# Performance work log

Measured on AMD Instinct MI355X. Metric: run time of the kernel, lower is better.

The kernel has to match this reference:

```python
import jax, jax.numpy as jnp
import numpy as np

# static sizes
B = 32          # graphs
NPER = 1024     # nodes per graph
N0 = B * NPER
F_IN = 128
H = 4           # heads
DH = 32         # per-head dim (128/4)
HID = H * DH    # 128
E = 524288      # edges (avg degree 16)
K1, K2, K3 = 512, 256, 128  # ceil(0.5*nper) per stage
NC = 10


def gcn_agg(h, src, dst, w, n):
    """GCNConv propagation: sym-normalized aggregation with self-loops.
    h: [n,F] already projected; w: [E] edge weight (0 for filtered edges)."""
    deg = jax.ops.segment_sum(w, dst, num_segments=n) + 1.0  # +1 self-loop
    dinv = jax.lax.rsqrt(deg)
    coef = dinv[src] * dinv[dst] * w                          # [E]
    agg = jax.ops.segment_sum(h[src] * coef[:, None], dst, num_segments=n)
    return agg + h / deg[:, None]  # self-loop term: dinv[i]^2 = 1/deg[i]


def mh_gcn(x, W, b, src, dst, w, n):
    """MAGPoolGCNLayer: per-head GCNConv (32->32), relu, concat heads."""
    h = jnp.einsum('nhd,hde->nhe', x.reshape(n, H, DH), W).reshape(n, HID)
    return jax.nn.relu(gcn_agg(h, src, dst, w, n) + b.reshape(HID))


def att_pool(x, src, dst, w, A, psW, psb, n, k):
    """MultiHeadAtt: standard att, complex score, concat pooling, global weight."""
    sub = x.reshape(n, H, DH)
    att = jnp.einsum('nhd,hd->nh', sub, A)            # per-head Linear(32,1)
    cat = (att[:, :, None] * sub).reshape(n, HID)     # score*sub, concat
    score = (gcn_agg(cat @ psW, src, dst, w, n) + psb)[:, 0]  # GCNConv(HID,1)
    nper = n // B
    _, idx = jax.lax.top_k(score.reshape(B, nper), k)  # per-graph topk
    perm = (idx + jnp.arange(B)[:, None] * nper).reshape(-1)
    xn = x[perm] * jnp.tanh(score[perm])[:, None]      # global att weighting
    # filter_adj: remap kept nodes, mask edges touching dropped nodes
    nmap = jnp.full((n,), -1, jnp.int32).at[perm].set(jnp.arange(B * k, dtype=jnp.int32))
    ns, nd = nmap[src], nmap[dst]
    wn = w * ((ns >= 0) & (nd >= 0)).astype(w.dtype)
    return xn, jnp.maximum(ns, 0), jnp.maximum(nd, 0), wn


def readout(x):
    # graphs are contiguous with equal node counts -> reshape readout
    xr = x.reshape(B, -1, x.shape[-1])
    return jnp.concatenate([xr.max(1), xr.mean(1)], axis=1)  # [B, 2*HID]


def setup_inputs():
    key = jax.random.key(0)
    ks = jax.random.split(key, 26)
    gid = jnp.repeat(jnp.arange(B, dtype=jnp.int32), E // B)
    src = jax.random.randint(ks[0], (E,), 0, NPER, dtype=jnp.int32) + gid * NPER
    dst = jax.random.randint(ks[1], (E,), 0, NPER, dtype=jnp.int32) + gid * NPER
    x = jax.random.normal(ks[2], (N0, F_IN), jnp.float32)
    s = 0.1
    def rn(k, shp):
        return jax.random.normal(k, shp, jnp.float32) * s
    return {
        'x': x, 'src': src, 'dst': dst,
        'W1': rn(ks[3], (H, DH, DH)), 'b1': rn(ks[4], (H, DH)), 'A1': rn(ks[5], (H, DH)),
        'ps1W': rn(ks[6], (HID, 1)), 'ps1b': rn(ks[7], (1,)),
        'W2': rn(ks[8], (H, DH, DH)), 'b2': rn(ks[9], (H, DH)), 'A2': rn(ks[10], (H, DH)),
        'ps2W': rn(ks[11], (HID, 1)), 'ps2b': rn(ks[12], (1,)),
        'W3': rn(ks[13], (H, DH, DH)), 'b3': rn(ks[14], (H, DH)), 'A3': rn(ks[15], (H, DH)),
        'ps3W': rn(ks[16], (HID, 1)), 'ps3b': rn(ks[17], (1,)),
        'l1W': rn(ks[18], (2 * HID, HID)), 'l1b': rn(ks[19], (HID,)),
        'l2W': rn(ks[20], (HID, HID // 2)), 'l2b': rn(ks[21], (HID // 2,)),
        'l3W': rn(ks[22], (HID // 2, NC)), 'l3b': rn(ks[23], (NC,)),
    }


def reference(x, src, dst, W1, b1, A1, ps1W, ps1b, W2, b2, A2, ps2W, ps2b,
              W3, b3, A3, ps3W, ps3b, l1W, l1b, l2W, l2b, l3W, l3b):
    w = jnp.ones((E,), x.dtype)
    h = mh_gcn(x, W1, b1, src, dst, w, N0)
    h, s1, d1, w1 = att_pool(h, src, dst, w, A1, ps1W, ps1b, N0, K1)
    r1 = readout(h)
    n1 = B * K1
    h = mh_gcn(h, W2, b2, s1, d1, w1, n1)
    h, s2, d2, w2 = att_pool(h, s1, d1, w1, A2, ps2W, ps2b, n1, K2)
    r2 = readout(h)
    n2 = B * K2
    h = mh_gcn(h, W3, b3, s2, d2, w2, n2)
    h, _, _, _ = att_pool(h, s2, d2, w2, A3, ps3W, ps3b, n2, K3)
    r3 = readout(h)
    z = r1 + r2 + r3                      # [B, 2*HID]
    z = jax.nn.relu(z @ l1W + l1b)        # dropout skipped (eval mode)
    z = jax.nn.relu(z @ l2W + l2b)
    return jax.nn.log_softmax(z @ l3W + l3b, axis=-1)
```

## Files before the change

### kernel.cpp

```cpp
#include <hip/hip_runtime.h>
#include <math.h>

#define BGR 32
#define NPER0 1024
#define N0 (BGR * NPER0)
#define FDIM 128
#define EDG 524288
#define K1 512
#define K2 256
#define K3 128
#define EBLK (EDG / 256)
#define SXP 36
#define CAP 64

__device__ __forceinline__ unsigned enc_f(float v) {
    unsigned u = __float_as_uint(v);
    return (u & 0x80000000u) ? ~u : (u | 0x80000000u);
}
__device__ __forceinline__ float dec_f(unsigned u) {
    return (u & 0x80000000u) ? __uint_as_float(u ^ 0x80000000u) : __uint_as_float(~u);
}

__global__ void zero_all(int* __restrict__ cntA, int* __restrict__ cntB,
                         int* __restrict__ cntC, unsigned* __restrict__ rmax,
                         float* __restrict__ rsum) {
    int i = blockIdx.x * 256 + threadIdx.x;
    if (i < N0) cntA[i] = 0;
    if (i < BGR * K1) cntB[i] = 0;
    if (i < BGR * K2) cntC[i] = 0;
    if (i < 3 * BGR * FDIM) { rmax[i] = 0u; rsum[i] = 0.0f; }
}

__device__ __forceinline__ void proj_compute(float* __restrict__ hp, int nb, int t,
                                             const float* __restrict__ sW,
                                             const float* __restrict__ sxT) {
    const int fg = t >> 3, ng = t & 7, h = fg >> 3;
    const float* ap = sxT + h * 32 * SXP + ng * 4;
    const float* bp = sW + h * 1024 + (fg & 7) * 4;
    float4 acc0 = {0.f, 0.f, 0.f, 0.f}, acc1 = acc0, acc2 = acc0, acc3 = acc0;
#pragma unroll
    for (int k = 0; k < 32; k++) {
        float4 a = *(const float4*)(ap + k * SXP);
        float4 b = *(const float4*)(bp + k * 32);
        acc0.x = fmaf(a.x, b.x, acc0.x); acc0.y = fmaf(a.x, b.y, acc0.y);
        acc0.z = fmaf(a.x, b.z, acc0.z); acc0.w = fmaf(a.x, b.w, acc0.w);
        acc1.x = fmaf(a.y, b.x, acc1.x); acc1.y = fmaf(a.y, b.y, acc1.y);
        acc1.z = fmaf(a.y, b.z, acc1.z); acc1.w = fmaf(a.y, b.w, acc1.w);
        acc2.x = fmaf(a.z, b.x, acc2.x); acc2.y = fmaf(a.z, b.y, acc2.y);
        acc2.z = fmaf(a.z, b.z, acc2.z); acc2.w = fmaf(a.z, b.w, acc2.w);
        acc3.x = fmaf(a.w, b.x, acc3.x); acc3.y = fmaf(a.w, b.y, acc3.y);
        acc3.z = fmaf(a.w, b.z, acc3.z); acc3.w = fmaf(a.w, b.w, acc3.w);
    }
    float4* op = (float4*)(hp + (size_t)(nb + ng * 4) * FDIM + fg * 4);
    op[0] = acc0; op[32] = acc1; op[64] = acc2; op[96] = acc3;
}

__device__ __forceinline__ void pool_body(const float* __restrict__ ha,
                                          const int* __restrict__ perm,
                                          const float* __restrict__ mult, int k, int pb,
                                          unsigned* __restrict__ rmax,
                                          float* __restrict__ rsum,
                                          float* __restrict__ smax,
                                          float* __restrict__ ssum) {
    const int t = threadIdx.x;
    const int g = pb & 31;
    const int c = pb >> 5;
    const int f = t & 127, half = t >> 7;
    const int base = g * k + c * 8;
    float vmax = -1e30f, vsum = 0.0f;
#pragma unroll
    for (int j0 = 0; j0 < 4; j0++) {
        int newid = base + half + j0 * 2;
        int old = perm[newid];
        float m = mult[newid];
        float v = ha[(size_t)old * FDIM + f] * m;
        vmax = fmaxf(vmax, v);
        vsum += v;
    }
    if (half) { smax[f] = vmax; ssum[f] = vsum; }
    __syncthreads();
    if (!half) {
        vmax = fmaxf(vmax, smax[f]);
        vsum += ssum[f];
        atomicMax(&rmax[g * FDIM + f], enc_f(vmax));
        atomicAdd(&rsum[g * FDIM + f], vsum);
    }
}

__global__ void bin_proj1(const int* __restrict__ src, const int* __restrict__ dst,
                          int* __restrict__ cnt, int* __restrict__ slot,
                          const float* __restrict__ x, const float* __restrict__ W,
                          float* __restrict__ hp) {
    __shared__ __align__(16) float sW[4096];
    __shared__ __align__(16) float sxT[128 * SXP];
    const int t = threadIdx.x;
    if (blockIdx.x < EBLK) {
        int e = blockIdx.x * 256 + t;
        int s = src[e];
        int d = dst[e];
        int p = atomicAdd(&cnt[d], 1);
        if (p < CAP) slot[d * CAP + p] = s;
        return;
    }
    const int nb = (blockIdx.x - EBLK) * 32;
    for (int i = t; i < 4096; i += 256) sW[i] = W[i];
    for (int i = t; i < 4096; i += 256) {
        int node = i >> 7, dim = i & 127;
        sxT[dim * SXP + node] = x[(size_t)(nb + node) * FDIM + dim];
    }
    __syncthreads();
    proj_compute(hp, nb, t, sW, sxT);
}

__global__ void bin_proj_pool(const int* __restrict__ src0, const int* __restrict__ dst0,
                              const int* __restrict__ nmapA, const int* __restrict__ nmapB,
                              int* __restrict__ cnt_next, int* __restrict__ slot_next,
                              const float* __restrict__ ha, const int* __restrict__ perm,
                              const float* __restrict__ mult, const float* __restrict__ W,
                              float* __restrict__ hp, int ntiles, int kprev,
                              unsigned* __restrict__ rmax, float* __restrict__ rsum) {
    __shared__ __align__(16) float sW[4096];
    __shared__ __align__(16) float sxT[128 * SXP];
    const int t = threadIdx.x;
    if (blockIdx.x < EBLK) {
        int e = blockIdx.x * 256 + t;
        int a = nmapA[src0[e]];
        int b = nmapA[dst0[e]];
        if (nmapB != nullptr) {
            a = (a >= 0) ? nmapB[a] : -1;
            b = (b >= 0) ? nmapB[b] : -1;
        }
        if (a >= 0 && b >= 0) {
            int p = atomicAdd(&cnt_next[b], 1);
            if (p < CAP) slot_next[b * CAP + p] = a;
        }
        return;
    }
    if (blockIdx.x >= EBLK + ntiles) {
        pool_body(ha, perm, mult, kprev, blockIdx.x - (EBLK + ntiles), rmax, rsum, sW, sW + 128);
        return;
    }
    const int nb = (blockIdx.x - EBLK) * 32;
    for (int i = t; i < 4096; i += 256) sW[i] = W[i];
    for (int i = t; i < 4096; i += 256) {
        int node = i >> 7, dim = i & 127;
        int newid = nb + node;
        sxT[dim * SXP + node] = ha[(size_t)perm[newid] * FDIM + dim] * mult[newid];
    }
    __syncthreads();
    proj_compute(hp, nb, t, sW, sxT);
}

__global__ void pool_kernel(const float* __restrict__ ha, const int* __restrict__ perm,
                            const float* __restrict__ mult, int k,
                            unsigned* __restrict__ rmax, float* __restrict__ rsum) {
    __shared__ float smax[128], ssum[128];
    pool_body(ha, perm, mult, k, blockIdx.x, rmax, rsum, smax, ssum);
}

__global__ void agg_kernel(const float* __restrict__ hp, const float* __restrict__ b,
                           const int* __restrict__ cnt, const int* __restrict__ slot,
                           const float* __restrict__ A, const float* __restrict__ psW,
                           float* __restrict__ ha, float* __restrict__ csd, int nper) {
    const int w = threadIdx.x >> 6;
    const int lane = threadIdx.x & 63;
    const int g = blockIdx.x & 31;
    const int chunk = blockIdx.x >> 5;
    const int i = g * nper + chunk * 4 + w;
    const int ci = cnt[i];
    const float di = rsqrtf((float)ci + 1.0f);
    const int c = min(ci, CAP);
    const float2* __restrict__ hp2 = (const float2*)hp;
    float2 self = hp2[(size_t)i * 64 + lane];
    float accx = self.x * di * di, accy = self.y * di * di;
    int idx = 0;
    float dv = 0.0f;
    if (lane < c) {
        idx = slot[i * CAP + lane];
        dv = rsqrtf((float)cnt[idx] + 1.0f);
    }
    int j = 0;
    for (; j + 3 < c; j += 4) {
        int s0 = __shfl(idx, j, 64);
        int s1 = __shfl(idx, j + 1, 64);
        int s2 = __shfl(idx, j + 2, 64);
        int s3 = __shfl(idx, j + 3, 64);
        float c0 = __shfl(dv, j, 64) * di;
        float c1 = __shfl(dv, j + 1, 64) * di;
        float c2 = __shfl(dv, j + 2, 64) * di;
        float c3 = __shfl(dv, j + 3, 64) * di;
        float2 v0 = hp2[(size_t)s0 * 64 + lane];
        float2 v1 = hp2[(size_t)s1 * 64 + lane];
        float2 v2 = hp2[(size_t)s2 * 64 + lane];
        float2 v3 = hp2[(size_t)s3 * 64 + lane];
        accx = fmaf(v0.x, c0, accx); accy = fmaf(v0.y, c0, accy);
        accx = fmaf(v1.x, c1, accx); accy = fmaf(v1.y, c1, accy);
        accx = fmaf(v2.x, c2, accx); accy = fmaf(v2.y, c2, accy);
        accx = fmaf(v3.x, c3, accx); accy = fmaf(v3.y, c3, accy);
    }
    for (; j < c; j++) {
        int s = __shfl(idx, j, 64);
        float co = __shfl(dv, j, 64) * di;
        float2 v = hp2[(size_t)s * 64 + lane];
        accx = fmaf(v.x, co, accx); accy = fmaf(v.y, co, accy);
    }
    float2 bb = ((const float2*)b)[lane];
    float2 o;
    o.x = fmaxf(accx + bb.x, 0.0f);
    o.y = fmaxf(accy + bb.y, 0.0f);
    ((float2*)ha)[(size_t)i * 64 + lane] = o;
    float2 Av = ((const float2*)A)[lane];
    float2 Pv = ((const float2*)psW)[lane];
    float a = o.x * Av.x + o.y * Av.y;
    float p = o.x * Pv.x + o.y * Pv.y;
#pragma unroll
    for (int d = 8; d > 0; d >>= 1) {
        a += __shfl_down(a, d, 16);
        p += __shfl_down(p, d, 16);
    }
    float part = a * p;
    part += __shfl_down(part, 16, 64);
    part += __shfl_down(part, 32, 64);
    if (lane == 0) csd[i] = part * di;
}

__global__ void topk_kernel(const float* __restrict__ csd, const int* __restrict__ cnt,
                            const int* __restrict__ slot, const float* __restrict__ psb,
                            int nper, int k, int* __restrict__ nmap, int* __restrict__ perm,
                            float* __restrict__ mult) {
    __shared__ float sc[NPER0];
    __shared__ unsigned ukey[NPER0];
    __shared__ unsigned hist[256];
    __shared__ unsigned wtot[4];
    __shared__ unsigned sel[2];
    __shared__ int ctr[2];
    const int g = blockIdx.x, t = threadIdx.x;
    const int w = t >> 6, l = t & 63;
    const int gnb = g * nper;
    const float pb = psb[0];
    const int Q = nper >> 8;
    {
        float acc[4] = {0.f, 0.f, 0.f, 0.f};
        float selfc[4] = {0.f, 0.f, 0.f, 0.f};
        float dl[4] = {0.f, 0.f, 0.f, 0.f};
        int nd[4] = {0, 0, 0, 0};
        int cc[4] = {0, 0, 0, 0};
        int m = 0;
#pragma unroll
        for (int q = 0; q < 4; q++) {
            if (q < Q) {
                int node = gnb + t + q * 256;
                int ci = cnt[node];
                nd[q] = node;
                cc[q] = min(ci, CAP);
                dl[q] = rsqrtf((float)ci + 1.0f);
                selfc[q] = csd[node];
                m = max(m, cc[q]);
            }
        }
        for (int j = 0; j < m; j++) {
#pragma unroll
            for (int q = 0; q < 4; q++) {
                if (q < Q && j < cc[q]) {
                    int s = slot[nd[q] * CAP + j];
                    acc[q] += csd[s];
                }
            }
        }
#pragma unroll
        for (int q = 0; q < 4; q++) {
            if (q < Q) {
                float v = dl[q] * (acc[q] + selfc[q]) + pb;
                sc[t + q * 256] = v;
                ukey[t + q * 256] = enc_f(v);
            }
        }
    }
    if (t == 0) { sel[0] = 0u; sel[1] = (unsigned)k; }
    __syncthreads();
    for (int shift = 24; shift >= 0; shift -= 8) {
        hist[t] = 0u;
        __syncthreads();
        const unsigned prefix = sel[0];
        const unsigned need = sel[1];
        for (int i = t; i < nper; i += 256) {
            unsigned u = ukey[i];
            if (shift == 24 || (u >> (shift + 8)) == (prefix >> (shift + 8)))
                atomicAdd(&hist[(u >> shift) & 255], 1u);
        }
        __syncthreads();
        const unsigned h = hist[t];
        unsigned s = h;
#pragma unroll
        for (int off = 1; off < 64; off <<= 1) {
            unsigned v = __shfl_down(s, off, 64);
            if (l + off < 64) s += v;
        }
        if (l == 0) wtot[w] = s;
        __syncthreads();
        unsigned add = 0;
        for (int ww = w + 1; ww < 4; ww++) add += wtot[ww];
        const unsigned sfx = s + add;
        const unsigned gtr = sfx - h;
        if (sfx >= need && gtr < need) {
            sel[0] = prefix | ((unsigned)t << shift);
            sel[1] = need - gtr;
        }
        __syncthreads();
    }
    const unsigned T = sel[0];
    const int need = (int)sel[1];
    if (t == 0) { ctr[0] = 0; ctr[1] = k - need; }
    __syncthreads();
    for (int i = t; i < nper; i += 256) {
        unsigned u = ukey[i];
        int node = gnb + i;
        int newid = -1;
        if (u > T) {
            newid = g * k + atomicAdd(&ctr[0], 1);
        } else if (u == T) {
            int slot2 = atomicAdd(&ctr[1], 1);
            if (slot2 < k) newid = g * k + slot2;
        }
        nmap[node] = newid;
        if (newid >= 0) {
            perm[newid] = node;
            mult[newid] = tanhf(sc[i]);
        }
    }
}

__global__ void final_mlp(const unsigned* __restrict__ rmax, const float* __restrict__ rsum,
                          const float* __restrict__ l1W, const float* __restrict__ l1b,
                          const float* __restrict__ l2W, const float* __restrict__ l2b,
                          const float* __restrict__ l3W, const float* __restrict__ l3b,
                          float* __restrict__ out) {
    __shared__ float sz[256], s1[128], s2[64], s3[10], red[2];
    const int g = blockIdx.x, t = threadIdx.x;
    const int RS = BGR * FDIM;
    sz[t] = dec_f(rmax[g * FDIM + t]) + dec_f(rmax[RS + g * FDIM + t]) +
            dec_f(rmax[2 * RS + g * FDIM + t]);
    sz[t + 128] = rsum[g * FDIM + t] / (float)K1 + rsum[RS + g * FDIM + t] / (float)K2 +
                  rsum[2 * RS + g * FDIM + t] / (float)K3;
    __syncthreads();
    float acc = l1b[t];
    for (int i = 0; i < 256; i++) acc = fmaf(sz[i], l1W[i * 128 + t], acc);
    s1[t] = fmaxf(acc, 0.0f);
    __syncthreads();
    if (t < 64) {
        float a2 = l2b[t];
        for (int i = 0; i < 128; i++) a2 = fmaf(s1[i], l2W[i * 64 + t], a2);
        s2[t] = fmaxf(a2, 0.0f);
    }
    __syncthreads();
    if (t < 10) {
        float a3 = l3b[t];
        for (int i = 0; i < 64; i++) a3 = fmaf(s2[i], l3W[i * 10 + t], a3);
        s3[t] = a3;
    }
    __syncthreads();
    if (t == 0) {
        float m = -1e30f;
        for (int c = 0; c < 10; c++) m = fmaxf(m, s3[c]);
        float sum = 0.0f;
        for (int c = 0; c < 10; c++) sum += expf(s3[c] - m);
        red[0] = m;
        red[1] = logf(sum);
    }
    __syncthreads();
    if (t < 10) out[g * 10 + t] = s3[t] - red[0] - red[1];
}

extern "C" void kernel_launch(void* const* d_in, const int* in_sizes, int n_in,
                              void* d_out, int out_size, void* d_ws, size_t ws_size,
                              hipStream_t stream) {
    const float* x    = (const float*)d_in[0];
    const int* src0   = (const int*)d_in[1];
    const int* dst0   = (const int*)d_in[2];
    const float* W1   = (const float*)d_in[3];
    const float* b1   = (const float*)d_in[4];
    const float* A1   = (const float*)d_in[5];
    const float* ps1W = (const float*)d_in[6];
    const float* ps1b = (const float*)d_in[7];
    const float* W2   = (const float*)d_in[8];
    const float* b2   = (const float*)d_in[9];
    const float* A2   = (const float*)d_in[10];
    const float* ps2W = (const float*)d_in[11];
    const float* ps2b = (const float*)d_in[12];
    const float* W3   = (const float*)d_in[13];
    const float* b3   = (const float*)d_in[14];
    const float* A3   = (const float*)d_in[15];
    const float* ps3W = (const float*)d_in[16];
    const float* ps3b = (const float*)d_in[17];
    const float* l1W  = (const float*)d_in[18];
    const float* l1b  = (const float*)d_in[19];
    const float* l2W  = (const float*)d_in[20];
    const float* l2b  = (const float*)d_in[21];
    const float* l3W  = (const float*)d_in[22];
    const float* l3b  = (const float*)d_in[23];
    float* out = (float*)d_out;

    char* ws = (char*)d_ws;
    size_t o = 0;
    auto alloc = [&](size_t bytes) -> void* {
        void* p = ws + o;
        o += (bytes + 255) & ~(size_t)255;
        return p;
    };
    float*    hproj = (float*)alloc((size_t)N0 * FDIM * 4);
    float*    hact  = (float*)alloc((size_t)N0 * FDIM * 4);
    int*      cntA  = (int*)alloc(N0 * 4);
    int*      cntB  = (int*)alloc(BGR * K1 * 4);
    int*      cntC  = (int*)alloc(BGR * K2 * 4);
    int*      slotA = (int*)alloc((size_t)N0 * CAP * 4);
    int*      slotB = (int*)alloc((size_t)BGR * K1 * CAP * 4);
    int*      slotC = (int*)alloc((size_t)BGR * K2 * CAP * 4);
    float*    cs    = (float*)alloc(N0 * 4);
    int*      nmapA = (int*)alloc(N0 * 4);
    int*      nmapB = (int*)alloc(BGR * K1 * 4);
    int*      nmapC = (int*)alloc(BGR * K2 * 4);
    int*      perm  = (int*)alloc(BGR * K1 * 4);
    float*    mult  = (float*)alloc(BGR * K1 * 4);
    unsigned* rmax  = (unsigned*)alloc(3 * BGR * FDIM * 4);
    float*    rsum  = (float*)alloc(3 * BGR * FDIM * 4);

    const int n1 = BGR * K1, n2 = BGR * K2;
    const int RS = BGR * FDIM;

    zero_all<<<N0 / 256, 256, 0, stream>>>(cntA, cntB, cntC, rmax, rsum);
    bin_proj1<<<EBLK + N0 / 32, 256, 0, stream>>>(src0, dst0, cntA, slotA, x, W1, hproj);
    agg_kernel<<<N0 / 4, 256, 0, stream>>>(hproj, b1, cntA, slotA, A1, ps1W, hact, cs, NPER0);
    topk_kernel<<<BGR, 256, 0, stream>>>(cs, cntA, slotA, ps1b, NPER0, K1, nmapA, perm, mult);

    bin_proj_pool<<<EBLK + n1 / 32 + BGR * K1 / 8, 256, 0, stream>>>(
        src0, dst0, nmapA, nullptr, cntB, slotB, hact, perm, mult, W2, hproj,
        n1 / 32, K1, rmax, rsum);
    agg_kernel<<<n1 / 4, 256, 0, stream>>>(hproj, b2, cntB, slotB, A2, ps2W, hact, cs, K1);
    topk_kernel<<<BGR, 256, 0, stream>>>(cs, cntB, slotB, ps2b, K1, K2, nmapB, perm, mult);

    bin_proj_pool<<<EBLK + n2 / 32 + BGR * K2 / 8, 256, 0, stream>>>(
        src0, dst0, nmapA, nmapB, cntC, slotC, hact, perm, mult, W3, hproj,
        n2 / 32, K2, rmax + RS, rsum + RS);
    agg_kernel<<<n2 / 4, 256, 0, stream>>>(hproj, b3, cntC, slotC, A3, ps3W, hact, cs, K2);
    topk_kernel<<<BGR, 256, 0, stream>>>(cs, cntC, slotC, ps3b, K2, K3, nmapC, perm, mult);

    pool_kernel<<<BGR * K3 / 8, 256, 0, stream>>>(hact, perm, mult, K3,
                                                  rmax + 2 * RS, rsum + 2 * RS);
    final_mlp<<<BGR, 128, 0, stream>>>(rmax, rsum, l1W, l1b, l2W, l2b, l3W, l3b, out);

    (void)in_sizes; (void)n_in; (void)out_size; (void)ws_size;
}
```

Baseline: 279.1 us.

## Compact adjacency slots per pooling stage and parallelize score gather

Each pooling stage now builds the next adjacency by compacting the previous stage's per-node neighbor slots with a wave ballot, instead of re-scanning all edges with atomics. The neighbor-score gather moves out of the 32-block topk kernel into a wide wave-per-node score_kernel. Histogram atomics in the radix select are pre-aggregated across the wave. Projection tiles are also reordered to interleave graphs. This removes the serialized per-graph gather and repeated full edge passes, at the cost of an extra launch and buffer, and it depends on the CAP truncation matching the earlier semantics.

```diff
diff --git a/kernel.cpp b/kernel.cpp
--- a/kernel.cpp
+++ b/kernel.cpp
@@ -21,13 +21,10 @@
     return (u & 0x80000000u) ? __uint_as_float(u ^ 0x80000000u) : __uint_as_float(~u);
 }
 
-__global__ void zero_all(int* __restrict__ cntA, int* __restrict__ cntB,
-                         int* __restrict__ cntC, unsigned* __restrict__ rmax,
+__global__ void zero_all(int* __restrict__ cntA, unsigned* __restrict__ rmax,
                          float* __restrict__ rsum) {
     int i = blockIdx.x * 256 + threadIdx.x;
     if (i < N0) cntA[i] = 0;
-    if (i < BGR * K1) cntB[i] = 0;
-    if (i < BGR * K2) cntC[i] = 0;
     if (i < 3 * BGR * FDIM) { rmax[i] = 0u; rsum[i] = 0.0f; }
 }
 
@@ -102,7 +99,8 @@
         if (p < CAP) slot[d * CAP + p] = s;
         return;
     }
-    const int nb = (blockIdx.x - EBLK) * 32;
+    const int tb = blockIdx.x - EBLK;
+    const int nb = (tb & 31) * NPER0 + (tb >> 5) * 32;
     for (int i = t; i < 4096; i += 256) sW[i] = W[i];
     for (int i = t; i < 4096; i += 256) {
         int node = i >> 7, dim = i & 127;
@@ -112,35 +110,39 @@
     proj_compute(hp, nb, t, sW, sxT);
 }
 
-__global__ void bin_proj_pool(const int* __restrict__ src0, const int* __restrict__ dst0,
-                              const int* __restrict__ nmapA, const int* __restrict__ nmapB,
+__global__ void bin_proj_pool(const int* __restrict__ cnt_prev,
+                              const int* __restrict__ slot_prev,
+                              const int* __restrict__ nmap,
                               int* __restrict__ cnt_next, int* __restrict__ slot_next,
                               const float* __restrict__ ha, const int* __restrict__ perm,
                               const float* __restrict__ mult, const float* __restrict__ W,
-                              float* __restrict__ hp, int ntiles, int kprev,
+                              float* __restrict__ hp, int ncomp, int ntiles, int kprev,
                               unsigned* __restrict__ rmax, float* __restrict__ rsum) {
     __shared__ __align__(16) float sW[4096];
     __shared__ __align__(16) float sxT[128 * SXP];
     const int t = threadIdx.x;
-    if (blockIdx.x < EBLK) {
-        int e = blockIdx.x * 256 + t;
-        int a = nmapA[src0[e]];
-        int b = nmapA[dst0[e]];
-        if (nmapB != nullptr) {
-            a = (a >= 0) ? nmapB[a] : -1;
-            b = (b >= 0) ? nmapB[b] : -1;
-        }
-        if (a >= 0 && b >= 0) {
-            int p = atomicAdd(&cnt_next[b], 1);
-            if (p < CAP) slot_next[b * CAP + p] = a;
-        }
+    if (blockIdx.x < ncomp) {
+        const int w = t >> 6, lane = t & 63;
+        const int b = (blockIdx.x & 31) * kprev + (blockIdx.x >> 5) * 4 + w;
+        const int old = perm[b];
+        const int c = min(cnt_prev[old], CAP);
+        int a = -1;
+        if (lane < c) a = nmap[slot_prev[(size_t)old * CAP + lane]];
+        unsigned long long mk = __ballot(a >= 0);
+        if (a >= 0) {
+            int pos = __popcll(mk & ((1ull << lane) - 1ull));
+            slot_next[(size_t)b * CAP + pos] = a;
+        }
+        if (lane == 0) cnt_next[b] = __popcll(mk);
         return;
     }
-    if (blockIdx.x >= EBLK + ntiles) {
-        pool_body(ha, perm, mult, kprev, blockIdx.x - (EBLK + ntiles), rmax, rsum, sW, sW + 128);
+    if (blockIdx.x >= ncomp + ntiles) {
+        pool_body(ha, perm, mult, kprev, blockIdx.x - (ncomp + ntiles), rmax, rsum,
+                  sW, sW + 128);
         return;
     }
-    const int nb = (blockIdx.x - EBLK) * 32;
+    const int tb = blockIdx.x - ncomp;
+    const int nb = (tb & 31) * kprev + (tb >> 5) * 32;
     for (int i = t; i < 4096; i += 256) sW[i] = W[i];
     for (int i = t; i < 4096; i += 256) {
         int node = i >> 7, dim = i & 127;
@@ -224,9 +226,26 @@
     if (lane == 0) csd[i] = part * di;
 }
 
-__global__ void topk_kernel(const float* __restrict__ csd, const int* __restrict__ cnt,
-                            const int* __restrict__ slot, const float* __restrict__ psb,
-                            int nper, int k, int* __restrict__ nmap, int* __restrict__ perm,
+__global__ void score_kernel(const float* __restrict__ csd, const int* __restrict__ cnt,
+                             const int* __restrict__ slot, const float* __restrict__ psb,
+                             float* __restrict__ scout, int nper) {
+    const int w = threadIdx.x >> 6;
+    const int lane = threadIdx.x & 63;
+    const int g = blockIdx.x & 31;
+    const int chunk = blockIdx.x >> 5;
+    const int i = g * nper + chunk * 4 + w;
+    const int ci = cnt[i];
+    const int c = min(ci, CAP);
+    float v = 0.0f;
+    if (lane < c) v = csd[slot[(size_t)i * CAP + lane]];
+#pragma unroll
+    for (int d = 32; d > 0; d >>= 1) v += __shfl_xor(v, d, 64);
+    if (lane == 0)
+        scout[i] = rsqrtf((float)ci + 1.0f) * (v + csd[i]) + psb[0];
+}
+
+__global__ void topk_kernel(const float* __restrict__ scin, int nper, int k,
+                            int* __restrict__ nmap, int* __restrict__ perm,
                             float* __restrict__ mult) {
     __shared__ float sc[NPER0];
     __shared__ unsigned ukey[NPER0];
@@ -237,44 +256,10 @@
     const int g = blockIdx.x, t = threadIdx.x;
     const int w = t >> 6, l = t & 63;
     const int gnb = g * nper;
-    const float pb = psb[0];
-    const int Q = nper >> 8;
-    {
-        float acc[4] = {0.f, 0.f, 0.f, 0.f};
-        float selfc[4] = {0.f, 0.f, 0.f, 0.f};
-        float dl[4] = {0.f, 0.f, 0.f, 0.f};
-        int nd[4] = {0, 0, 0, 0};
-        int cc[4] = {0, 0, 0, 0};
-        int m = 0;
-#pragma unroll
-        for (int q = 0; q < 4; q++) {
-            if (q < Q) {
-                int node = gnb + t + q * 256;
-                int ci = cnt[node];
-                nd[q] = node;
-                cc[q] = min(ci, CAP);
-                dl[q] = rsqrtf((float)ci + 1.0f);
-                selfc[q] = csd[node];
-                m = max(m, cc[q]);
-            }
-        }
-        for (int j = 0; j < m; j++) {
-#pragma unroll
-            for (int q = 0; q < 4; q++) {
-                if (q < Q && j < cc[q]) {
-                    int s = slot[nd[q] * CAP + j];
-                    acc[q] += csd[s];
-                }
-            }
-        }
-#pragma unroll
-        for (int q = 0; q < 4; q++) {
-            if (q < Q) {
-                float v = dl[q] * (acc[q] + selfc[q]) + pb;
-                sc[t + q * 256] = v;
-                ukey[t + q * 256] = enc_f(v);
-            }
-        }
+    for (int i = t; i < nper; i += 256) {
+        float v = scin[gnb + i];
+        sc[i] = v;
+        ukey[i] = enc_f(v);
     }
     if (t == 0) { sel[0] = 0u; sel[1] = (unsigned)k; }
     __syncthreads();
@@ -285,8 +270,16 @@
         const unsigned need = sel[1];
         for (int i = t; i < nper; i += 256) {
             unsigned u = ukey[i];
-            if (shift == 24 || (u >> (shift + 8)) == (prefix >> (shift + 8)))
-                atomicAdd(&hist[(u >> shift) & 255], 1u);
+            bool inp = (shift == 24) || ((u >> (shift + 8)) == (prefix >> (shift + 8)));
+            int dig = inp ? (int)((u >> shift) & 255u) : -1;
+            int cv = inp ? 1 : 0;
+#pragma unroll
+            for (int d = 1; d < 64; d <<= 1) {
+                int od = __shfl_xor(dig, d, 64);
+                int oc = __shfl_xor(cv, d, 64);
+                if (od == dig) cv = ((l & d) == 0) ? (cv + oc) : 0;
+            }
+            if (dig >= 0 && cv > 0) atomicAdd(&hist[dig], (unsigned)cv);
         }
         __syncthreads();
         const unsigned h = hist[t];
@@ -416,6 +409,7 @@
     int*      slotB = (int*)alloc((size_t)BGR * K1 * CAP * 4);
     int*      slotC = (int*)alloc((size_t)BGR * K2 * CAP * 4);
     float*    cs    = (float*)alloc(N0 * 4);
+    float*    scb   = (float*)alloc(N0 * 4);
     int*      nmapA = (int*)alloc(N0 * 4);
     int*      nmapB = (int*)alloc(BGR * K1 * 4);
     int*      nmapC = (int*)alloc(BGR * K2 * 4);
@@ -427,22 +421,25 @@
     const int n1 = BGR * K1, n2 = BGR * K2;
     const int RS = BGR * FDIM;
 
-    zero_all<<<N0 / 256, 256, 0, stream>>>(cntA, cntB, cntC, rmax, rsum);
+    zero_all<<<N0 / 256, 256, 0, stream>>>(cntA, rmax, rsum);
     bin_proj1<<<EBLK + N0 / 32, 256, 0, stream>>>(src0, dst0, cntA, slotA, x, W1, hproj);
     agg_kernel<<<N0 / 4, 256, 0, stream>>>(hproj, b1, cntA, slotA, A1, ps1W, hact, cs, NPER0);
-    topk_kernel<<<BGR, 256, 0, stream>>>(cs, cntA, slotA, ps1b, NPER0, K1, nmapA, perm, mult);
-
-    bin_proj_pool<<<EBLK + n1 / 32 + BGR * K1 / 8, 256, 0, stream>>>(
-        src0, dst0, nmapA, nullptr, cntB, slotB, hact, perm, mult, W2, hproj,
-        n1 / 32, K1, rmax, rsum);
+    score_kernel<<<N0 / 4, 256, 0, stream>>>(cs, cntA, slotA, ps1b, scb, NPER0);
+    topk_kernel<<<BGR, 256, 0, stream>>>(scb, NPER0, K1, nmapA, perm, mult);
+
+    bin_proj_pool<<<n1 / 4 + n1 / 32 + BGR * K1 / 8, 256, 0, stream>>>(
+        cntA, slotA, nmapA, cntB, slotB, hact, perm, mult, W2, hproj,
+        n1 / 4, n1 / 32, K1, rmax, rsum);
     agg_kernel<<<n1 / 4, 256, 0, stream>>>(hproj, b2, cntB, slotB, A2, ps2W, hact, cs, K1);
-    topk_kernel<<<BGR, 256, 0, stream>>>(cs, cntB, slotB, ps2b, K1, K2, nmapB, perm, mult);
-
-    bin_proj_pool<<<EBLK + n2 / 32 + BGR * K2 / 8, 256, 0, stream>>>(
-        src0, dst0, nmapA, nmapB, cntC, slotC, hact, perm, mult, W3, hproj,
-        n2 / 32, K2, rmax + RS, rsum + RS);
+    score_kernel<<<n1 / 4, 256, 0, stream>>>(cs, cntB, slotB, ps2b, scb, K1);
+    topk_kernel<<<BGR, 256, 0, stream>>>(scb, K1, K2, nmapB, perm, mult);
+
+    bin_proj_pool<<<n2 / 4 + n2 / 32 + BGR * K2 / 8, 256, 0, stream>>>(
+        cntB, slotB, nmapB, cntC, slotC, hact, perm, mult, W3, hproj,
+        n2 / 4, n2 / 32, K2, rmax + RS, rsum + RS);
     agg_kernel<<<n2 / 4, 256, 0, stream>>>(hproj, b3, cntC, slotC, A3, ps3W, hact, cs, K2);
-    topk_kernel<<<BGR, 256, 0, stream>>>(cs, cntC, slotC, ps3b, K2, K3, nmapC, perm, mult);
+    score_kernel<<<n2 / 4, 256, 0, stream>>>(cs, cntC, slotC, ps3b, scb, K2);
+    topk_kernel<<<BGR, 256, 0, stream>>>(scb, K2, K3, nmapC, perm, mult);
 
     pool_kernel<<<BGR * K3 / 8, 256, 0, stream>>>(hact, perm, mult, K3,
                                                   rmax + 2 * RS, rsum + 2 * RS);
```

New measurement: 253.3 us. 1.1x faster.
